# Performance work log

Hardware: AMD Instinct MI355X
Metric: run time of the kernel (lower is better)

Reference implementation:

```python
import jax, jax.numpy as jnp
import numpy as np

N_NODES = 50000
N_EDGES = 800000
MUL = 16            # multiplicity of each irrep (16x0e + 16x1o)
RADIAL_IN = 8       # radial basis size
RADIAL_HID = 64
N_PATHS = 5         # TP paths: s*Y0->s, v.Yv->s, s*Yv->v, v*Y0->v, v x Yv->v
NUM_SPECIES = 4
AVG_NEIGH = 16.0


def setup_inputs() -> dict:
    key = jax.random.key(0)
    ks = jax.random.split(key, 16)
    inp = {
        'node_scalars': jax.random.normal(ks[0], (N_NODES, MUL), jnp.float32),
        'node_vectors': jax.random.normal(ks[1], (N_NODES, MUL * 3), jnp.float32),
        'edge_sh': jax.random.normal(ks[2], (N_EDGES, 4), jnp.float32),
        'radial_emb': jax.random.uniform(ks[3], (N_EDGES, RADIAL_IN), jnp.float32),
        'senders': jax.random.randint(ks[4], (N_EDGES,), 0, N_NODES, jnp.int32),
        'receivers': jax.random.randint(ks[5], (N_EDGES,), 0, N_NODES, jnp.int32),
        'species': jax.random.randint(ks[6], (N_NODES,), 0, NUM_SPECIES, jnp.int32),
        # learned params (fan-in scaled)
        'W_in_s': jax.random.normal(ks[7], (MUL, MUL), jnp.float32) / np.sqrt(MUL),
        'W_in_v': jax.random.normal(ks[8], (MUL, MUL), jnp.float32) / np.sqrt(MUL),
        'mlp_w1': jax.random.normal(ks[9], (RADIAL_IN, RADIAL_HID), jnp.float32) / np.sqrt(RADIAL_IN),
        'mlp_b1': jnp.zeros((RADIAL_HID,), jnp.float32),
        'mlp_w2': jax.random.normal(ks[10], (RADIAL_HID, N_PATHS * MUL), jnp.float32) / np.sqrt(RADIAL_HID),
        'W_out_s': jax.random.normal(ks[11], (2 * MUL, 2 * MUL), jnp.float32) / np.sqrt(2 * MUL),
        'W_out_v': jax.random.normal(ks[12], (3 * MUL, MUL), jnp.float32) / np.sqrt(3 * MUL),
        'sc_s': jax.random.normal(ks[13], (NUM_SPECIES, MUL, 2 * MUL), jnp.float32) / np.sqrt(MUL),
        'sc_v': jax.random.normal(ks[14], (NUM_SPECIES, MUL, MUL), jnp.float32) / np.sqrt(MUL),
    }
    return inp


def reference(node_scalars, node_vectors, edge_sh, radial_emb, senders, receivers,
              species, W_in_s, W_in_v, mlp_w1, mlp_b1, mlp_w2, W_out_s, W_out_v,
              sc_s, sc_v):
    N = node_scalars.shape[0]
    inv_sqrt_deg = 1.0 / np.sqrt(AVG_NEIGH)

    # ---- input per-irrep linear ----
    s = node_scalars @ W_in_s                                  # [N,16]
    v_in = node_vectors.reshape(N, MUL, 3)
    v = jnp.einsum('nuc,uw->nwc', v_in, W_in_v)                # [N,16,3]

    # ---- gather sender features ----
    xs = s[senders]                                            # [E,16]
    xv = v[senders]                                            # [E,16,3]
    Y0 = edge_sh[:, :1]                                        # [E,1] l=0 SH
    Yv = edge_sh[:, 1:4]                                       # [E,3] l=1 SH

    # ---- radial MLP -> per-path tensor-product weights ----
    h = jax.nn.silu(radial_emb @ mlp_w1 + mlp_b1)              # [E,64]
    w = (h @ mlp_w2).reshape(-1, N_PATHS, MUL)                 # [E,5,16]

    # ---- CG tensor product (uvu) messages ----
    m_s1 = w[:, 0] * xs * Y0                                   # 0e x 0e -> 0e
    m_s2 = w[:, 1] * jnp.einsum('euc,ec->eu', xv, Yv)          # 1o x 1o -> 0e (dot)
    m_v1 = w[:, 2, :, None] * xs[:, :, None] * Yv[:, None, :]  # 0e x 1o -> 1o
    m_v2 = w[:, 3, :, None] * xv * Y0[:, :, None]              # 1o x 0e -> 1o
    m_v3 = w[:, 4, :, None] * jnp.cross(xv, Yv[:, None, :])    # 1o x 1o -> 1o (cross)

    # ---- scatter-sum to receivers + neighbour normalization ----
    m_s = jnp.concatenate([m_s1, m_s2], axis=-1)               # [E,32]
    m_v = jnp.concatenate([m_v1, m_v2, m_v3], axis=1)          # [E,48,3]
    a_s = jax.ops.segment_sum(m_s, receivers, num_segments=N) * inv_sqrt_deg
    a_v = jax.ops.segment_sum(m_v, receivers, num_segments=N) * inv_sqrt_deg

    # ---- output per-irrep linear ----
    pre_s = a_s @ W_out_s                                      # [N,32]
    pre_v = jnp.einsum('nuc,uw->nwc', a_v, W_out_v)            # [N,16,3]

    # ---- species-dependent self connection ----
    pre_s = pre_s + jnp.einsum('nu,nuw->nw', node_scalars, sc_s[species])
    pre_v = pre_v + jnp.einsum('nuc,nuw->nwc', v_in, sc_v[species])

    # ---- gate nonlinearity ----
    out_s = jax.nn.silu(pre_s[:, :MUL])                        # scalar outputs
    gates = jax.nn.sigmoid(pre_s[:, MUL:])                     # gate scalars
    out_v = pre_v * gates[:, :, None]

    # ---- resnet ----
    out_s = out_s + node_scalars
    out_v = out_v + v_in

    return jnp.concatenate([out_s, out_v.reshape(N, MUL * 3)], axis=-1)
```

## Files before the change

### kernel.cpp

```cpp
#include <hip/hip_runtime.h>
#include <hip/hip_bf16.h>

typedef unsigned short u16;
typedef unsigned int   u32;
typedef _Float16 h2 __attribute__((ext_vector_type(2)));
typedef short s8v __attribute__((ext_vector_type(8)));
typedef float f4v __attribute__((ext_vector_type(4)));

#define N_NODES 50000
#define N_EDGES 800000
#define NCH   4
#define RPC   12500
#define CHMAX 204800

#define RPB   250
#define NBINS 200
#define EPB   4096
#define NBB   ((N_EDGES+EPB-1)/EPB)

#define WB_W1H  0
#define WB_B1   256
#define WB_W2F  320
#define WB_WINS 2880
#define WB_WINV 3136
#define WB_WOS  3392
#define WB_WOV  4416
#define WB_SCS  5184
#define WB_SCV  7232
#define WB_FLAG 8256
#define OFF_SP16 8260
#define OFF_VP16 408260
#define IDX_BCNT 1608260
#define IDX_BOF2 1608516
#define IDX_BCUR 1608772
#define IDX_OFFS 1658260
#define IDX_BUCK 1758262
#define OFF_WP   2558264
#define ACC_OFF  10750272
#define IDX_EEID 12950400
#define OFF_ER16 13750400

__device__ __forceinline__ float bf2f(u16 v){
  union { u32 u; float f; } x; x.u = ((u32)v) << 16; return x.f;
}
__device__ __forceinline__ u16 f2bf(float f){
  u32 u = __float_as_uint(f);
  u32 lsb = (u >> 16) & 1u;
  u32 r = u + 0x7fffu + lsb;
  return (u16)(r >> 16);
}
__device__ __forceinline__ float ldx(const void* p, long long i, int isf){
  return isf ? ((const float*)p)[i] : bf2f(((const u16*)p)[i]);
}
__device__ __forceinline__ u32 pkh2(float a, float b){
  union { u32 u; h2 v; } x; x.v.x = (_Float16)a; x.v.y = (_Float16)b; return x.u;
}
__device__ __forceinline__ float dot2(h2 a, u32 w, float c){
  union { u32 u; h2 v; } x; x.u = w;
#if __has_builtin(__builtin_amdgcn_fdot2)
  return __builtin_amdgcn_fdot2(a, x.v, c, false);
#else
  return c + (float)a.x*(float)x.v.x + (float)a.y*(float)x.v.y;
#endif
}
__device__ __forceinline__ float sigmoidf_(float x){ return 1.f/(1.f + __expf(-x)); }

__global__ void detect_dtype(const u32* __restrict__ remb_raw, int* __restrict__ flag){
  int isf32 = 0;
  for (int k = 0; k < 64; k++){
    u32 w = remb_raw[k];
    u32 lo = w & 0xffffu, hi = w >> 16;
    int okl = ((lo & 0x8000u) == 0) && (((lo >> 7) & 0xffu) <= 126u);
    int okh = ((hi & 0x8000u) == 0) && (((hi >> 7) & 0xffu) <= 126u);
    if (!(okl && okh)) isf32 = 1;
  }
  *flag = isf32;
}

__global__ void prep_weights(const void* __restrict__ w1, const void* __restrict__ b1g,
                             const void* __restrict__ w2, const void* __restrict__ wins,
                             const void* __restrict__ winv, const void* __restrict__ wos,
                             const void* __restrict__ wov, const void* __restrict__ scs,
                             const void* __restrict__ scv, float* __restrict__ wbuf,
                             const int* __restrict__ flag){
  int t = threadIdx.x;
  int isf = *flag;
  u32* w1h  = (u32*)(wbuf + WB_W1H);
  u16* w2f  = (u16*)(wbuf + WB_W2F);
  for (int idx=t; idx<256;  idx+=256){
    int j = idx>>2, ip = idx&3;
    w1h[idx] = pkh2(ldx(w1, (2*ip)*64+j, isf), ldx(w1, (2*ip+1)*64+j, isf));
  }
  for (int idx=t; idx<64;   idx+=256){ wbuf[WB_B1+idx]  = ldx(b1g, idx, isf); }
  for (int idx=t; idx<5120; idx+=256){
    int tt = idx >> 10;
    int rem = idx & 1023;
    int kh = rem >> 9;
    int rem2 = rem & 511;
    int ln = rem2 >> 3, j = rem2 & 7;
    int k = kh*32 + (ln>>4)*8 + j;
    int o = tt*16 + (ln&15);
    w2f[idx] = f2bf(ldx(w2, (long long)k*80 + o, isf));
  }
  for (int idx=t; idx<256;  idx+=256){ wbuf[WB_WINS+idx] = ldx(wins, idx, isf); }
  for (int idx=t; idx<256;  idx+=256){ wbuf[WB_WINV+idx] = ldx(winv, idx, isf); }
  for (int idx=t; idx<1024; idx+=256){ wbuf[WB_WOS+idx]  = ldx(wos, idx, isf); }
  for (int idx=t; idx<768;  idx+=256){ wbuf[WB_WOV+idx]  = ldx(wov, idx, isf); }
  for (int idx=t; idx<2048; idx+=256){ wbuf[WB_SCS+idx]  = ldx(scs, idx, isf); }
  for (int idx=t; idx<1024; idx+=256){ wbuf[WB_SCV+idx]  = ldx(scv, idx, isf); }
}

__global__ void node_pre(const void* __restrict__ ns_g, const void* __restrict__ nv_g,
                         const float* __restrict__ wbuf, u16* __restrict__ sp16,
                         u16* __restrict__ vp16, const int* __restrict__ flag){
  int n = blockIdx.x*256 + threadIdx.x;
  if (n >= N_NODES) return;
  int isf = *flag;
  float a[16], b[48];
  #pragma unroll
  for (int u=0;u<16;u++) a[u] = ldx(ns_g, n*16+u, isf);
  #pragma unroll
  for (int u=0;u<48;u++) b[u] = ldx(nv_g, n*48+u, isf);
  const float* wins = wbuf + WB_WINS;
  const float* winv = wbuf + WB_WINV;
  float s[16];
  #pragma unroll
  for (int w=0;w<16;w++) s[w]=0.f;
  #pragma unroll
  for (int u=0;u<16;u++){
    float au = a[u];
    #pragma unroll
    for (int w=0;w<16;w++) s[w] += au * wins[u*16+w];
  }
  #pragma unroll
  for (int w=0;w<16;w++) sp16[n*16+w] = f2bf(s[w]);
  float v0[16], v1[16], v2[16];
  #pragma unroll
  for (int w=0;w<16;w++){ v0[w]=0.f; v1[w]=0.f; v2[w]=0.f; }
  #pragma unroll
  for (int u=0;u<16;u++){
    float bu0=b[u*3], bu1=b[u*3+1], bu2=b[u*3+2];
    #pragma unroll
    for (int w=0;w<16;w++){
      float wv = winv[u*16+w];
      v0[w] += bu0*wv; v1[w] += bu1*wv; v2[w] += bu2*wv;
    }
  }
  #pragma unroll
  for (int w=0;w<16;w++){
    vp16[n*48+w*3]   = f2bf(v0[w]);
    vp16[n*48+w*3+1] = f2bf(v1[w]);
    vp16[n*48+w*3+2] = f2bf(v2[w]);
  }
}

__global__ void __launch_bounds__(256) bin_count(const int* __restrict__ receivers,
                                                 int* __restrict__ bcnt){
  __shared__ int lcnt[NBINS];
  int t = threadIdx.x;
  for (int i=t;i<NBINS;i+=256) lcnt[i]=0;
  __syncthreads();
  int base = blockIdx.x*EPB;
  for (int i=t;i<EPB;i+=256){
    int e = base+i;
    if (e<N_EDGES) atomicAdd(&lcnt[receivers[e]/RPB],1);
  }
  __syncthreads();
  for (int i=t;i<NBINS;i+=256) if (lcnt[i]) atomicAdd(&bcnt[i], lcnt[i]);
}

__global__ void bin_scan(const int* __restrict__ bcnt, int* __restrict__ binoff,
                         int* __restrict__ bincur, int* __restrict__ offs){
  __shared__ int lds[NBINS];
  int t=threadIdx.x;
  if (t<NBINS) lds[t]=bcnt[t];
  __syncthreads();
  for (int off=1; off<NBINS; off<<=1){
    int v = (t<NBINS && t>=off)? lds[t-off] : 0;
    __syncthreads();
    if (t<NBINS) lds[t]+=v;
    __syncthreads();
  }
  if (t<NBINS){ int ex = lds[t]-bcnt[t]; binoff[t]=ex; bincur[t]=ex; }
  if (t==0) offs[N_NODES] = N_EDGES;
}

__global__ void __launch_bounds__(256) bin_scatter(const int* __restrict__ receivers,
                 int* __restrict__ bincur, u32* __restrict__ eeid, u16* __restrict__ er){
  __shared__ int lcnt[NBINS], loff[NBINS], lcur[NBINS], gbase[NBINS];
  __shared__ u32 seid[EPB];
  __shared__ u16 sr[EPB];
  int t = threadIdx.x;
  for (int i=t;i<NBINS;i+=256) lcnt[i]=0;
  __syncthreads();
  int base = blockIdx.x*EPB;
  int r_[16];
  #pragma unroll
  for (int k=0;k<16;k++){
    int e = base + t + k*256;
    r_[k] = (e<N_EDGES)? receivers[e] : -1;
    if (r_[k]>=0) atomicAdd(&lcnt[r_[k]/RPB],1);
  }
  __syncthreads();
  if (t<NBINS) loff[t]=lcnt[t];
  __syncthreads();
  for (int off=1; off<NBINS; off<<=1){
    int v=(t<NBINS&&t>=off)?loff[t-off]:0;
    __syncthreads();
    if (t<NBINS) loff[t]+=v;
    __syncthreads();
  }
  if (t<NBINS){
    int ex=loff[t]-lcnt[t]; loff[t]=ex; lcur[t]=ex;
    gbase[t] = lcnt[t] ? atomicAdd(&bincur[t], lcnt[t]) : 0;
  }
  __syncthreads();
  #pragma unroll
  for (int k=0;k<16;k++){
    if (r_[k]>=0){
      int b=r_[k]/RPB;
      int p=atomicAdd(&lcur[b],1);
      seid[p]=(u32)(base + t + k*256);
      sr[p]=(u16)r_[k];
    }
  }
  __syncthreads();
  int rem = N_EDGES - base;
  int tot = rem < EPB ? rem : EPB;
  for (int i=t;i<tot;i+=256){
    int b = sr[i]/RPB;
    int dst = gbase[b] + (i - loff[b]);
    eeid[dst]=seid[i]; er[dst]=sr[i];
  }
}

__global__ void __launch_bounds__(256) bin_finalize(const u32* __restrict__ eeid,
        const u16* __restrict__ er, const int* __restrict__ binoff,
        const int* __restrict__ bcnt, int* __restrict__ offs, int* __restrict__ bucket){
  __shared__ int deg[RPB], pfx[RPB], lcur[RPB];
  int b=blockIdx.x, t=threadIdx.x;
  int beg=binoff[b], cnt=bcnt[b];
  for (int i=t;i<RPB;i+=256) deg[i]=0;
  __syncthreads();
  int r0=b*RPB;
  for (int i=t;i<cnt;i+=256) atomicAdd(&deg[er[beg+i]-r0],1);
  __syncthreads();
  if (t<RPB) pfx[t]=deg[t];
  __syncthreads();
  for (int off=1; off<RPB; off<<=1){
    int v=(t<RPB&&t>=off)?pfx[t-off]:0;
    __syncthreads();
    if (t<RPB) pfx[t]+=v;
    __syncthreads();
  }
  if (t<RPB){
    int ex=pfx[t]-deg[t]; pfx[t]=ex; lcur[t]=ex;
    offs[r0+t]=beg+ex;
  }
  __syncthreads();
  for (int i=t;i<cnt;i+=256){
    int rr = er[beg+i]-r0;
    int k = atomicAdd(&lcur[rr],1);
    bucket[beg+k] = (int)eeid[beg+i];
  }
}

__global__ void __launch_bounds__(256) pass1_w(
    const int* __restrict__ bucket, const int* __restrict__ offs,
    const void* __restrict__ remb, const float* __restrict__ wbuf,
    u16* __restrict__ wp16, int rlo, const int* __restrict__ flag){
  __shared__ u16 hlds[4*16*72];
  int tid = threadIdx.x;
  int lane = tid & 63, wid = tid >> 6;
  int isf = *flag;
  int chunkBeg = offs[rlo], chunkEnd = offs[rlo + RPC];
  int r0e = chunkBeg + (blockIdx.x*4 + wid)*16;
  if (r0e >= chunkEnd) return;
  u16* hw = hlds + wid*(16*72);
  int e = lane & 15, q = lane >> 4;

  int er = r0e + e;
  int eid = (er < chunkEnd) ? bucket[er] : 0;
  float re[8];
  #pragma unroll
  for (int i=0;i<8;i++) re[i] = ldx(remb, (long long)eid*8+i, isf);
  h2 reh[4];
  #pragma unroll
  for (int ip=0;ip<4;ip++){ reh[ip].x=(_Float16)re[2*ip]; reh[ip].y=(_Float16)re[2*ip+1]; }
  const u32* w1h = (const u32*)(wbuf + WB_W1H);
  const float* b1 = wbuf + WB_B1;
  #pragma unroll
  for (int jj=0;jj<16;jj++){
    int j = q*16 + jj;
    float a = b1[j];
    #pragma unroll
    for (int ip=0;ip<4;ip++) a = dot2(reh[ip], w1h[j*4+ip], a);
    a = a * sigmoidf_(a);
    hw[e*72 + j] = f2bf(a);
  }
  asm volatile("s_waitcnt lgkmcnt(0)" ::: "memory");

  const u16* w2f = (const u16*)(wbuf + WB_W2F);
  s8v bfr[5][2];
  #pragma unroll
  for (int t=0;t<5;t++)
    #pragma unroll
    for (int kh=0;kh<2;kh++)
      bfr[t][kh] = *(const s8v*)(w2f + ((t*2+kh)*64 + lane)*8);

  f4v acc[5];
  #pragma unroll
  for (int t=0;t<5;t++) acc[t] = (f4v){0.f,0.f,0.f,0.f};
  #pragma unroll
  for (int kh=0;kh<2;kh++){
    s8v af = *(const s8v*)(hw + e*72 + kh*32 + q*8);
    #pragma unroll
    for (int t=0;t<5;t++)
      acc[t] = __builtin_amdgcn_mfma_f32_16x16x32_bf16(af, bfr[t][kh], acc[t], 0,0,0);
  }
  int n = lane & 15;
  #pragma unroll
  for (int r=0;r<4;r++){
    int er2 = r0e + q*4 + r;
    if (er2 < chunkEnd){
      int widx = er2 - chunkBeg;
      #pragma unroll
      for (int t=0;t<5;t++)
        wp16[(size_t)t*(CHMAX*16) + (size_t)widx*16 + n] = f2bf(acc[t][r]);
    }
  }
}

__global__ void __launch_bounds__(256, 4) pass2_reduce(
    const int* __restrict__ bucket, const int* __restrict__ offs,
    const void* __restrict__ edge_sh, const int* __restrict__ senders,
    const u16* __restrict__ sp16, const u16* __restrict__ vp16,
    const u16* __restrict__ wp16, float* __restrict__ accbuf,
    int rlo, const int* __restrict__ flag){
  int tid = threadIdx.x;
  int lane = tid & 63, wid = tid >> 6;
  int u = lane & 15, q = lane >> 4;
  int isf = *flag;
  int r = rlo + blockIdx.x*4 + wid;
  int chunkBeg = offs[rlo];
  int beg = offs[r], end = offs[r+1];
  float As0=0.f,As1=0.f;
  float Av00=0.f,Av01=0.f,Av02=0.f, Av10=0.f,Av11=0.f,Av12=0.f, Av20=0.f,Av21=0.f,Av22=0.f;
  for (int rank = beg + q; rank < end; rank += 4){
    int eid = bucket[rank];
    float Y0  = ldx(edge_sh,(long long)eid*4+0,isf);
    float Yv0 = ldx(edge_sh,(long long)eid*4+1,isf);
    float Yv1 = ldx(edge_sh,(long long)eid*4+2,isf);
    float Yv2 = ldx(edge_sh,(long long)eid*4+3,isf);
    int snd = senders[eid];
    size_t widx = (size_t)(rank - chunkBeg)*16 + u;
    float w0 = bf2f(wp16[widx]);
    float w1 = bf2f(wp16[(size_t)1*(CHMAX*16) + widx]);
    float w2 = bf2f(wp16[(size_t)2*(CHMAX*16) + widx]);
    float w3 = bf2f(wp16[(size_t)3*(CHMAX*16) + widx]);
    float w4 = bf2f(wp16[(size_t)4*(CHMAX*16) + widx]);
    float xs = bf2f(sp16[(size_t)snd*16 + u]);
    float x0 = bf2f(vp16[(size_t)snd*48 + u*3 + 0]);
    float x1 = bf2f(vp16[(size_t)snd*48 + u*3 + 1]);
    float x2 = bf2f(vp16[(size_t)snd*48 + u*3 + 2]);
    As0 += w0*xs*Y0;
    As1 += w1*(x0*Yv0 + x1*Yv1 + x2*Yv2);
    float t1 = w2*xs;  Av00 += t1*Yv0; Av01 += t1*Yv1; Av02 += t1*Yv2;
    float t2 = w3*Y0;  Av10 += t2*x0;  Av11 += t2*x1;  Av12 += t2*x2;
    Av20 += w4*(x1*Yv2 - x2*Yv1);
    Av21 += w4*(x2*Yv0 - x0*Yv2);
    Av22 += w4*(x0*Yv1 - x1*Yv0);
  }
  #define RED2(x) { x += __shfl_xor(x,16); x += __shfl_xor(x,32); }
  RED2(As0) RED2(As1)
  RED2(Av00) RED2(Av01) RED2(Av02)
  RED2(Av10) RED2(Av11) RED2(Av12)
  RED2(Av20) RED2(Av21) RED2(Av22)
  #undef RED2
  float* ab = accbuf + (size_t)(r - rlo)*176;
  if (q == 0){ ab[u]=As0;    ab[32+u]=Av00;  ab[112+u]=Av21; }
  else if (q == 1){ ab[16+u]=As1; ab[80+u]=Av01;  ab[144+u]=Av12; }
  else if (q == 2){ ab[48+u]=Av10; ab[128+u]=Av02; ab[160+u]=Av22; }
  else            { ab[64+u]=Av20; ab[96+u]=Av11; }
}

__global__ void __launch_bounds__(256) pass2_epilogue(
    const float* __restrict__ accbuf, const float* __restrict__ wbuf,
    const void* __restrict__ ns_g, const void* __restrict__ nv_g,
    const int* __restrict__ species, void* __restrict__ out,
    int rlo, const int* __restrict__ flag){
  __shared__ float sb[16*176 + 16*16 + 16*48];
  int tid = threadIdx.x;
  int isf = *flag;
  int n0 = rlo + blockIdx.x*16;
  int rem = rlo + RPC - n0;
  int nblk = rem < 16 ? rem : 16;
  {
    int tot = nblk*176;
    const float* src = accbuf + (size_t)(n0 - rlo)*176;
    for (int i=tid; i<tot; i+=256) sb[i] = src[i];
    float* nsb = sb + 2816;
    for (int i=tid; i<nblk*16; i+=256)
      nsb[i] = ldx(ns_g, (long long)n0*16 + i, isf);
    float* vinb = sb + 2816 + 256;
    for (int i=tid; i<nblk*48; i+=256)
      vinb[i] = ldx(nv_g, (long long)n0*48 + i, isf);
  }
  __syncthreads();
  int g = tid >> 4, u = tid & 15;
  if (g >= nblk) return;
  int nn = n0 + g;
  const float* bin  = sb + g*176;
  const float* nsb  = sb + 2816 + g*16;
  const float* vinb = sb + 2816 + 256 + g*48;
  int sp = species[nn];
  const float* wos = wbuf + WB_WOS;
  const float* scs = wbuf + WB_SCS + sp*512;
  const float* wov = wbuf + WB_WOV;
  const float* scv = wbuf + WB_SCV + sp*256;
  float p0 = 0.f, p1 = 0.f;
  #pragma unroll
  for (int j=0;j<32;j++){
    float a = bin[j]*0.25f;
    p0 += a*wos[j*32+u];
    p1 += a*wos[j*32+16+u];
  }
  #pragma unroll
  for (int j=0;j<16;j++){
    float nu = nsb[j];
    p0 += nu*scs[j*32+u];
    p1 += nu*scs[j*32+16+u];
  }
  float gate = sigmoidf_(p1);
  float os = p0*sigmoidf_(p0) + nsb[u];
  float pv0, pv1, pv2;
  {
    float a0=0.f, a1=0.f, a2=0.f;
    #pragma unroll
    for (int j=0;j<48;j++){
      float wv = wov[j*16+u];
      a0 += bin[32 + 0*48 + j]*0.25f*wv;
      a1 += bin[32 + 1*48 + j]*0.25f*wv;
      a2 += bin[32 + 2*48 + j]*0.25f*wv;
    }
    #pragma unroll
    for (int j=0;j<16;j++){
      float sv = scv[j*16+u];
      a0 += vinb[j*3+0]*sv;
      a1 += vinb[j*3+1]*sv;
      a2 += vinb[j*3+2]*sv;
    }
    pv0 = a0*gate + vinb[u*3+0];
    pv1 = a1*gate + vinb[u*3+1];
    pv2 = a2*gate + vinb[u*3+2];
  }
  if (isf){
    float* orow = (float*)out + (size_t)nn*64;
    orow[u] = os;
    orow[16 + u*3 + 0] = pv0;
    orow[16 + u*3 + 1] = pv1;
    orow[16 + u*3 + 2] = pv2;
  } else {
    u16* orow = (u16*)out + (size_t)nn*64;
    orow[u] = f2bf(os);
    orow[16 + u*3 + 0] = f2bf(pv0);
    orow[16 + u*3 + 1] = f2bf(pv1);
    orow[16 + u*3 + 2] = f2bf(pv2);
  }
}

extern "C" void kernel_launch(void* const* d_in, const int* in_sizes, int n_in,
                              void* d_out, int out_size, void* d_ws, size_t ws_size,
                              hipStream_t stream){
  const void* node_scalars = d_in[0];
  const void* node_vectors = d_in[1];
  const void* edge_sh      = d_in[2];
  const void* radial_emb   = d_in[3];
  const int* senders      = (const int*)d_in[4];
  const int* receivers    = (const int*)d_in[5];
  const int* species      = (const int*)d_in[6];
  const void* W_in_s  = d_in[7];
  const void* W_in_v  = d_in[8];
  const void* mlp_w1  = d_in[9];
  const void* mlp_b1  = d_in[10];
  const void* mlp_w2  = d_in[11];
  const void* W_out_s = d_in[12];
  const void* W_out_v = d_in[13];
  const void* sc_s    = d_in[14];
  const void* sc_v    = d_in[15];

  float* wsf  = (float*)d_ws;
  int*   wsi  = (int*)d_ws;
  u32*   wsu  = (u32*)d_ws;
  float* wbuf = wsf;
  u16*   sp16 = (u16*)(wsu + OFF_SP16);
  u16*   vp16 = (u16*)(wsu + OFF_VP16);
  int*   bcnt = wsi + IDX_BCNT;
  int*   bof2 = wsi + IDX_BOF2;
  int*   bcur = wsi + IDX_BCUR;
  int*   offs = wsi + IDX_OFFS;
  int*   buck = wsi + IDX_BUCK;
  u16*   wp16 = (u16*)(wsu + OFF_WP);
  float* accb = wsf + ACC_OFF;
  u32*   eeid = wsu + IDX_EEID;
  u16*   er16 = (u16*)(wsu + OFF_ER16);
  int*   flag = (int*)(wbuf + WB_FLAG);

  detect_dtype<<<1,1,0,stream>>>((const u32*)radial_emb, flag);
  hipMemsetAsync(bcnt, 0, NBINS*sizeof(int), stream);
  prep_weights<<<1,256,0,stream>>>(mlp_w1, mlp_b1, mlp_w2, W_in_s, W_in_v,
                                   W_out_s, W_out_v, sc_s, sc_v, wbuf, flag);
  node_pre<<<(N_NODES+255)/256,256,0,stream>>>(node_scalars, node_vectors, wbuf,
                                               sp16, vp16, flag);
  bin_count<<<NBB,256,0,stream>>>(receivers, bcnt);
  bin_scan<<<1,256,0,stream>>>(bcnt, bof2, bcur, offs);
  bin_scatter<<<NBB,256,0,stream>>>(receivers, bcur, eeid, er16);
  bin_finalize<<<NBINS,256,0,stream>>>(eeid, er16, bof2, bcnt, offs, buck);
  for (int c = 0; c < NCH; c++){
    int rlo = c * RPC;
    pass1_w<<<CHMAX/64, 256, 0, stream>>>(buck, offs, radial_emb, wbuf, wp16, rlo, flag);
    pass2_reduce<<<RPC/4, 256, 0, stream>>>(buck, offs, edge_sh, senders,
                                            sp16, vp16, wp16, accb, rlo, flag);
    pass2_epilogue<<<(RPC+15)/16, 256, 0, stream>>>(accb, wbuf, node_scalars,
                                                    node_vectors, species,
                                                    d_out, rlo, flag);
  }
}
```

Measured before the change: 453.9 us.

## Interleave node features and edge weights for vectorized gathers in pass2

Packs projected node scalars and vector components into one interleaved 4-wide bf16 record per channel, and stores the five per-edge path weights as one padded 8-wide record instead of five separate planes. The gathers in pass2_reduce and the loads of edge_sh and radial_emb become single vector loads. The reduction loop is also unrolled by two. The padding raises the write and read footprint of the weight buffer by 3 wasted slots per entry.

```diff
diff --git a/kernel.cpp b/kernel.cpp
--- a/kernel.cpp
+++ b/kernel.cpp
@@ -6,6 +6,7 @@
 typedef _Float16 h2 __attribute__((ext_vector_type(2)));
 typedef short s8v __attribute__((ext_vector_type(8)));
 typedef float f4v __attribute__((ext_vector_type(4)));
+typedef u16 u16x4 __attribute__((ext_vector_type(4)));
 
 #define N_NODES 50000
 #define N_EDGES 800000
@@ -28,17 +29,16 @@
 #define WB_SCS  5184
 #define WB_SCV  7232
 #define WB_FLAG 8256
-#define OFF_SP16 8260
-#define OFF_VP16 408260
+#define OFF_SV16 8260
 #define IDX_BCNT 1608260
 #define IDX_BOF2 1608516
 #define IDX_BCUR 1608772
 #define IDX_OFFS 1658260
 #define IDX_BUCK 1758262
 #define OFF_WP   2558264
-#define ACC_OFF  10750272
-#define IDX_EEID 12950400
-#define OFF_ER16 13750400
+#define ACC_OFF  15665472
+#define IDX_EEID 17865472
+#define OFF_ER16 18665472
 
 __device__ __forceinline__ float bf2f(u16 v){
   union { u32 u; float f; } x; x.u = ((u32)v) << 16; return x.f;
@@ -111,8 +111,8 @@
 }
 
 __global__ void node_pre(const void* __restrict__ ns_g, const void* __restrict__ nv_g,
-                         const float* __restrict__ wbuf, u16* __restrict__ sp16,
-                         u16* __restrict__ vp16, const int* __restrict__ flag){
+                         const float* __restrict__ wbuf, u16* __restrict__ sv16,
+                         const int* __restrict__ flag){
   int n = blockIdx.x*256 + threadIdx.x;
   if (n >= N_NODES) return;
   int isf = *flag;
@@ -132,8 +132,6 @@
     #pragma unroll
     for (int w=0;w<16;w++) s[w] += au * wins[u*16+w];
   }
-  #pragma unroll
-  for (int w=0;w<16;w++) sp16[n*16+w] = f2bf(s[w]);
   float v0[16], v1[16], v2[16];
   #pragma unroll
   for (int w=0;w<16;w++){ v0[w]=0.f; v1[w]=0.f; v2[w]=0.f; }
@@ -146,11 +144,12 @@
       v0[w] += bu0*wv; v1[w] += bu1*wv; v2[w] += bu2*wv;
     }
   }
+  u16x4* svp = (u16x4*)sv16 + (size_t)n*16;
   #pragma unroll
   for (int w=0;w<16;w++){
-    vp16[n*48+w*3]   = f2bf(v0[w]);
-    vp16[n*48+w*3+1] = f2bf(v1[w]);
-    vp16[n*48+w*3+2] = f2bf(v2[w]);
+    u16x4 pk;
+    pk[0]=f2bf(s[w]); pk[1]=f2bf(v0[w]); pk[2]=f2bf(v1[w]); pk[3]=f2bf(v2[w]);
+    svp[w] = pk;
   }
 }
 
@@ -282,8 +281,16 @@
   int er = r0e + e;
   int eid = (er < chunkEnd) ? bucket[er] : 0;
   float re[8];
-  #pragma unroll
-  for (int i=0;i<8;i++) re[i] = ldx(remb, (long long)eid*8+i, isf);
+  if (isf){
+    f4v ra = ((const f4v*)remb)[(size_t)eid*2];
+    f4v rb = ((const f4v*)remb)[(size_t)eid*2+1];
+    re[0]=ra[0]; re[1]=ra[1]; re[2]=ra[2]; re[3]=ra[3];
+    re[4]=rb[0]; re[5]=rb[1]; re[6]=rb[2]; re[7]=rb[3];
+  } else {
+    s8v r8 = ((const s8v*)remb)[eid];
+    #pragma unroll
+    for (int i=0;i<8;i++) re[i] = bf2f((u16)r8[i]);
+  }
   h2 reh[4];
   #pragma unroll
   for (int ip=0;ip<4;ip++){ reh[ip].x=(_Float16)re[2*ip]; reh[ip].y=(_Float16)re[2*ip+1]; }
@@ -323,10 +330,12 @@
   for (int r=0;r<4;r++){
     int er2 = r0e + q*4 + r;
     if (er2 < chunkEnd){
-      int widx = er2 - chunkBeg;
-      #pragma unroll
-      for (int t=0;t<5;t++)
-        wp16[(size_t)t*(CHMAX*16) + (size_t)widx*16 + n] = f2bf(acc[t][r]);
+      size_t widx = (size_t)(er2 - chunkBeg);
+      s8v pk;
+      pk[0]=(short)f2bf(acc[0][r]); pk[1]=(short)f2bf(acc[1][r]);
+      pk[2]=(short)f2bf(acc[2][r]); pk[3]=(short)f2bf(acc[3][r]);
+      pk[4]=(short)f2bf(acc[4][r]); pk[5]=0; pk[6]=0; pk[7]=0;
+      *(s8v*)(wp16 + (widx*16 + n)*8) = pk;
     }
   }
 }
@@ -334,9 +343,8 @@
 __global__ void __launch_bounds__(256, 4) pass2_reduce(
     const int* __restrict__ bucket, const int* __restrict__ offs,
     const void* __restrict__ edge_sh, const int* __restrict__ senders,
-    const u16* __restrict__ sp16, const u16* __restrict__ vp16,
-    const u16* __restrict__ wp16, float* __restrict__ accbuf,
-    int rlo, const int* __restrict__ flag){
+    const u16* __restrict__ sv16, const u16* __restrict__ wp16,
+    float* __restrict__ accbuf, int rlo, const int* __restrict__ flag){
   int tid = threadIdx.x;
   int lane = tid & 63, wid = tid >> 6;
   int u = lane & 15, q = lane >> 4;
@@ -346,23 +354,22 @@
   int beg = offs[r], end = offs[r+1];
   float As0=0.f,As1=0.f;
   float Av00=0.f,Av01=0.f,Av02=0.f, Av10=0.f,Av11=0.f,Av12=0.f, Av20=0.f,Av21=0.f,Av22=0.f;
-  for (int rank = beg + q; rank < end; rank += 4){
+  auto body = [&](int rank){
     int eid = bucket[rank];
-    float Y0  = ldx(edge_sh,(long long)eid*4+0,isf);
-    float Yv0 = ldx(edge_sh,(long long)eid*4+1,isf);
-    float Yv1 = ldx(edge_sh,(long long)eid*4+2,isf);
-    float Yv2 = ldx(edge_sh,(long long)eid*4+3,isf);
+    float Y0,Yv0,Yv1,Yv2;
+    if (isf){
+      f4v y = ((const f4v*)edge_sh)[eid];
+      Y0=y[0]; Yv0=y[1]; Yv1=y[2]; Yv2=y[3];
+    } else {
+      u16x4 y = ((const u16x4*)edge_sh)[eid];
+      Y0=bf2f(y[0]); Yv0=bf2f(y[1]); Yv1=bf2f(y[2]); Yv2=bf2f(y[3]);
+    }
     int snd = senders[eid];
-    size_t widx = (size_t)(rank - chunkBeg)*16 + u;
-    float w0 = bf2f(wp16[widx]);
-    float w1 = bf2f(wp16[(size_t)1*(CHMAX*16) + widx]);
-    float w2 = bf2f(wp16[(size_t)2*(CHMAX*16) + widx]);
-    float w3 = bf2f(wp16[(size_t)3*(CHMAX*16) + widx]);
-    float w4 = bf2f(wp16[(size_t)4*(CHMAX*16) + widx]);
-    float xs = bf2f(sp16[(size_t)snd*16 + u]);
-    float x0 = bf2f(vp16[(size_t)snd*48 + u*3 + 0]);
-    float x1 = bf2f(vp16[(size_t)snd*48 + u*3 + 1]);
-    float x2 = bf2f(vp16[(size_t)snd*48 + u*3 + 2]);
+    s8v wv = *(const s8v*)(wp16 + ((size_t)(rank - chunkBeg)*16 + u)*8);
+    float w0=bf2f((u16)wv[0]), w1=bf2f((u16)wv[1]), w2=bf2f((u16)wv[2]);
+    float w3=bf2f((u16)wv[3]), w4=bf2f((u16)wv[4]);
+    u16x4 sv = *(const u16x4*)(sv16 + ((size_t)snd*16 + u)*4);
+    float xs=bf2f(sv[0]), x0=bf2f(sv[1]), x1=bf2f(sv[2]), x2=bf2f(sv[3]);
     As0 += w0*xs*Y0;
     As1 += w1*(x0*Yv0 + x1*Yv1 + x2*Yv2);
     float t1 = w2*xs;  Av00 += t1*Yv0; Av01 += t1*Yv1; Av02 += t1*Yv2;
@@ -370,7 +377,10 @@
     Av20 += w4*(x1*Yv2 - x2*Yv1);
     Av21 += w4*(x2*Yv0 - x0*Yv2);
     Av22 += w4*(x0*Yv1 - x1*Yv0);
-  }
+  };
+  int rank = beg + q;
+  for (; rank + 4 < end; rank += 8){ body(rank); body(rank+4); }
+  if (rank < end) body(rank);
   #define RED2(x) { x += __shfl_xor(x,16); x += __shfl_xor(x,32); }
   RED2(As0) RED2(As1)
   RED2(Av00) RED2(Av01) RED2(Av02)
@@ -493,8 +503,7 @@
   int*   wsi  = (int*)d_ws;
   u32*   wsu  = (u32*)d_ws;
   float* wbuf = wsf;
-  u16*   sp16 = (u16*)(wsu + OFF_SP16);
-  u16*   vp16 = (u16*)(wsu + OFF_VP16);
+  u16*   sv16 = (u16*)(wsu + OFF_SV16);
   int*   bcnt = wsi + IDX_BCNT;
   int*   bof2 = wsi + IDX_BOF2;
   int*   bcur = wsi + IDX_BCUR;
@@ -511,7 +520,7 @@
   prep_weights<<<1,256,0,stream>>>(mlp_w1, mlp_b1, mlp_w2, W_in_s, W_in_v,
                                    W_out_s, W_out_v, sc_s, sc_v, wbuf, flag);
   node_pre<<<(N_NODES+255)/256,256,0,stream>>>(node_scalars, node_vectors, wbuf,
-                                               sp16, vp16, flag);
+                                               sv16, flag);
   bin_count<<<NBB,256,0,stream>>>(receivers, bcnt);
   bin_scan<<<1,256,0,stream>>>(bcnt, bof2, bcur, offs);
   bin_scatter<<<NBB,256,0,stream>>>(receivers, bcur, eeid, er16);
@@ -520,7 +529,7 @@
     int rlo = c * RPC;
     pass1_w<<<CHMAX/64, 256, 0, stream>>>(buck, offs, radial_emb, wbuf, wp16, rlo, flag);
     pass2_reduce<<<RPC/4, 256, 0, stream>>>(buck, offs, edge_sh, senders,
-                                            sp16, vp16, wp16, accb, rlo, flag);
+                                            sv16, wp16, accb, rlo, flag);
     pass2_epilogue<<<(RPC+15)/16, 256, 0, stream>>>(accb, wbuf, node_scalars,
                                                     node_vectors, species,
                                                     d_out, rlo, flag);
```

Result: no change. 446.0 us (-1.7%).
